# Kernel optimization log

Hardware: AMD Instinct MI355X
Metric: run time of the kernel (lower is better)

## Reference

```python
import jax, jax.numpy as jnp
import numpy as np

B, L, H, T, C = 4, 256, 768, 16, 6
SIM_THR = 0.0
EPS_LN = 1e-5


def layer_norm(x, g, b):
    m = x.mean(-1, keepdims=True)
    v = ((x - m) ** 2).mean(-1, keepdims=True)
    return (x - m) / jnp.sqrt(v + EPS_LN) * g + b


def setup_inputs() -> dict:
    key = jax.random.key(0)
    ks = jax.random.split(key, 20)
    s = 0.02
    embeddings = jax.random.normal(ks[0], (B, L, H), jnp.float32)
    masks = jnp.ones((B, L, L), jnp.float32)
    asp_st = jax.random.randint(ks[1], (B, T), 0, 12)
    asp_ed = asp_st + jax.random.randint(ks[2], (B, T), 0, 3)
    opi_st = jax.random.randint(ks[3], (B, T), 0, 12)
    opi_ed = opi_st + jax.random.randint(ks[4], (B, T), 0, 3)
    sent_id = jax.random.randint(ks[5], (B, T), 2, 5)
    return {
        "embeddings": embeddings, "masks": masks,
        "asp_st": asp_st, "asp_ed": asp_ed, "opi_st": opi_st, "opi_ed": opi_ed,
        "sent_id": sent_id,
        "edge_embed": jax.random.normal(ks[6], (2, H), jnp.float32) * s,
        "W_tp": jax.random.normal(ks[7], (2 * H + 3, H), jnp.float32) * s,
        "b_tp": jnp.zeros((H,), jnp.float32),
        "W_attn": jax.random.normal(ks[8], (3 * H, 1), jnp.float32) * s,
        "b_attn": jnp.zeros((1,), jnp.float32),
        "W_gat": jax.random.normal(ks[9], (2 * H, H), jnp.float32) * s,
        "b_gat": jnp.zeros((H,), jnp.float32),
        "gamma0": jnp.ones((H,), jnp.float32), "beta0": jnp.zeros((H,), jnp.float32),
        "W1": jax.random.normal(ks[10], (2 * H, L), jnp.float32) * s,
        "bl1": jnp.zeros((L,), jnp.float32),
        "gamma1": jnp.ones((L,), jnp.float32), "beta1": jnp.zeros((L,), jnp.float32),
        "Wc": jax.random.normal(ks[11], (L, C), jnp.float32) * s,
        "bc": jnp.zeros((C,), jnp.float32),
        "Wc1": jax.random.normal(ks[12], (L, 2), jnp.float32) * s,
        "bc1": jnp.zeros((2,), jnp.float32),
    }


def _triplet_enhance(emb_b, a_st, a_ed, o_st, o_ed, sid,
                     edge_embed, W_tp, b_tp, W_attn, b_attn, W_gat, b_gat):
    # emb_b: [L,H]; span ints: [T]
    pos = jnp.arange(L)
    am = (pos[None, :] >= a_st[:, None]) & (pos[None, :] <= a_ed[:, None])  # [T,L]
    om = (pos[None, :] >= o_st[:, None]) & (pos[None, :] <= o_ed[:, None])
    amf = am.astype(emb_b.dtype)
    omf = om.astype(emb_b.dtype)
    asp = (amf @ emb_b) / amf.sum(1, keepdims=True)  # [T,H] span-mean
    opi = (omf @ emb_b) / omf.sum(1, keepdims=True)
    sv = jax.nn.one_hot(sid - 2, 3, dtype=emb_b.dtype)  # [T,3]
    nf = jnp.concatenate([asp, opi, sv], -1) @ W_tp + b_tp  # [T,H]

    # cosine similarity between triplet nodes
    nrm = nf / jnp.maximum(jnp.linalg.norm(nf, axis=-1, keepdims=True), 1e-8)
    sim = nrm @ nrm.T
    eye = jnp.eye(T, dtype=bool)
    ok = (sim > SIM_THR) & ~eye
    m0 = ok & (a_st[:, None] == a_st[None, :]) & (a_ed[:, None] == a_ed[None, :])
    m1 = ok & (o_st[:, None] == o_st[None, :]) & (o_ed[:, None] == o_ed[None, :])
    # edge (i,j): src=i, tgt=j -> incoming mask indexed [tgt, src, etype]
    emask = jnp.stack([m0.T, m1.T], axis=-1)  # [T,T,2]

    E = edge_embed  # [2,H]
    cc = jnp.concatenate([
        jnp.broadcast_to(nf[:, None, None, :], (T, T, 2, H)),   # target feats
        jnp.broadcast_to(nf[None, :, None, :], (T, T, 2, H)),   # source feats
        jnp.broadcast_to(E[None, None, :, :], (T, T, 2, H)),
    ], -1)  # [T,T,2,3H]
    scores = (jax.nn.leaky_relu(cc, 0.2) @ W_attn)[..., 0] + b_attn[0]  # [T,T,2]
    neg = jnp.where(emask, scores, -1e9)
    attn = jax.nn.softmax(neg.reshape(T, -1), axis=-1).reshape(T, T, 2)
    msg = jnp.concatenate([
        jnp.broadcast_to(nf[:, None, :], (T, 2, H)),
        jnp.broadcast_to(E[None, :, :], (T, 2, H)),
    ], -1)  # [src, etype, 2H]
    agg = jnp.einsum('tse,sef->tf', attn, msg)
    upd = jax.nn.relu(agg @ W_gat + b_gat)
    has_in = emask.any(axis=(1, 2))
    new_nf = jnp.where(has_in[:, None], upd, nf)
    has_edges = emask.any().astype(emb_b.dtype)  # original skips scatter if no edges
    center = (a_st + o_st) // 2
    return emb_b.at[center].add(new_nf * has_edges)


def reference(embeddings, masks, asp_st, asp_ed, opi_st, opi_ed, sent_id,
              edge_embed, W_tp, b_tp, W_attn, b_attn, W_gat, b_gat,
              gamma0, beta0, W1, bl1, gamma1, beta1, Wc, bc, Wc1, bc1):
    emb1 = layer_norm(embeddings, gamma0, beta0)
    emb = jax.vmap(_triplet_enhance,
                   in_axes=(0, 0, 0, 0, 0, 0) + (None,) * 7)(
        emb1, asp_st, asp_ed, opi_st, opi_ed, sent_id,
        edge_embed, W_tp, b_tp, W_attn, b_attn, W_gat, b_gat)

    # cat([feat_exp, feat_expT]) @ W1  ==  emb@W1[:H] (rows) + emb@W1[H:] (cols)
    A = jnp.einsum('bih,hk->bik', emb, W1[:H])
    Bm = jnp.einsum('bjh,hk->bjk', emb, W1[H:])
    hidden = A[:, :, None, :] + Bm[:, None, :, :] + bl1  # [B,L,L,L]
    hidden = jax.nn.gelu(layer_norm(hidden, gamma1, beta1), approximate=False)
    logits = (hidden @ Wc + bc) * masks[..., None]    # [B,L,L,C]
    logits1 = (hidden @ Wc1 + bc1) * masks[..., None]  # [B,L,L,2]
    return jnp.concatenate([logits, logits1], -1)
```

## Files before the change

kernel.cpp:

```cpp
#include <hip/hip_runtime.h>

__device__ __forceinline__ unsigned short f2bf(float f) {
    union { float f; unsigned u; } v; v.f = f;
    unsigned u = v.u;
    unsigned r = (u + 0x7fffu + ((u >> 16) & 1u)) >> 16;
    return (unsigned short)r;
}
__device__ __forceinline__ float blo(unsigned u) {
    union { unsigned v; float f; } x; x.v = u << 16; return x.f;
}
__device__ __forceinline__ float bhi(unsigned u) {
    union { unsigned v; float f; } x; x.v = u & 0xffff0000u; return x.f;
}

typedef __attribute__((ext_vector_type(8))) short short8;
typedef __attribute__((ext_vector_type(4))) float floatx4;

#define Bn 4
#define Ln 256
#define Hn 768
#define Tn 16

__global__ __launch_bounds__(256) void k_ln0(const float* __restrict__ x,
                                             const float* __restrict__ g,
                                             const float* __restrict__ be,
                                             float* __restrict__ out) {
    int row = blockIdx.x, tid = threadIdx.x;
    const float* xr = x + (size_t)row * Hn;
    float v0 = xr[tid], v1 = xr[tid + 256], v2 = xr[tid + 512];
    float s = v0 + v1 + v2;
    float q = v0 * v0 + v1 * v1 + v2 * v2;
    __shared__ float sm[4], qm[4];
    for (int o = 32; o > 0; o >>= 1) { s += __shfl_down(s, o); q += __shfl_down(q, o); }
    if ((tid & 63) == 0) { sm[tid >> 6] = s; qm[tid >> 6] = q; }
    __syncthreads();
    float S = sm[0] + sm[1] + sm[2] + sm[3];
    float Q = qm[0] + qm[1] + qm[2] + qm[3];
    float mean = S * (1.f / 768.f);
    float rstd = rsqrtf(Q * (1.f / 768.f) - mean * mean + 1e-5f);
    float* o0 = out + (size_t)row * Hn;
    o0[tid]       = (v0 - mean) * rstd * g[tid]       + be[tid];
    o0[tid + 256] = (v1 - mean) * rstd * g[tid + 256] + be[tid + 256];
    o0[tid + 512] = (v2 - mean) * rstd * g[tid + 512] + be[tid + 512];
}

__global__ __launch_bounds__(256) void k_spans(const float* __restrict__ emb,
                                               const int* __restrict__ ast_, const int* __restrict__ aed_,
                                               const int* __restrict__ ost_, const int* __restrict__ oed_,
                                               const int* __restrict__ sid_,
                                               float* __restrict__ xv,
                                               float* __restrict__ nf) {
    int n = blockIdx.x, b = n >> 4, tid = threadIdx.x;
    int ast = ast_[n], aed = aed_[n], ost = ost_[n], oed = oed_[n], sid = sid_[n];
    float ai = 1.f / (float)(aed - ast + 1);
    float oi = 1.f / (float)(oed - ost + 1);
    const float* eb = emb + (size_t)b * Ln * Hn;
    float* xr = xv + (size_t)n * 1568;
    for (int r = tid; r < 1568; r += 256) {
        float v;
        if (r < 768) {
            float s = 0.f;
            for (int l = ast; l <= aed; ++l) s += eb[l * Hn + r];
            v = s * ai;
        } else if (r < 1536) {
            int h = r - 768;
            float s = 0.f;
            for (int l = ost; l <= oed; ++l) s += eb[l * Hn + h];
            v = s * oi;
        } else if (r < 1539) {
            v = (sid - 2 == r - 1536) ? 1.f : 0.f;
        } else {
            v = 0.f;
        }
        xr[r] = v;
    }
    float* nr = nf + (size_t)n * Hn;
    nr[tid] = 0.f; nr[tid + 256] = 0.f; nr[tid + 512] = 0.f;
}

__global__ __launch_bounds__(256) void k_skinny(const float* __restrict__ A,
                                                const float* __restrict__ B,
                                                const float* __restrict__ bias,
                                                float* __restrict__ C,
                                                int Kpad, int Kb, int Kc) {
    __shared__ float At[32][33], Bt[32][33];
    int tid = threadIdx.x;
    int n0 = blockIdx.x * 32, m0 = blockIdx.y * 32, z = blockIdx.z;
    int kbeg = z * Kc;
    int kend = kbeg + Kc; if (kend > Kpad) kend = Kpad;
    int lr = tid >> 3, lc = (tid & 7) * 4;
    int tm = tid >> 3, tn4 = (tid & 7) * 4;
    float acc0 = 0.f, acc1 = 0.f, acc2 = 0.f, acc3 = 0.f;
    for (int k0 = kbeg; k0 < kend; k0 += 32) {
        float4 av = *(const float4*)(A + (size_t)(m0 + lr) * Kpad + k0 + lc);
        At[lr][lc] = av.x; At[lr][lc + 1] = av.y; At[lr][lc + 2] = av.z; At[lr][lc + 3] = av.w;
        int gk = k0 + lr;
        float4 bv = {0.f, 0.f, 0.f, 0.f};
        if (gk < Kb) bv = *(const float4*)(B + (size_t)gk * 768 + n0 + lc);
        Bt[lr][lc] = bv.x; Bt[lr][lc + 1] = bv.y; Bt[lr][lc + 2] = bv.z; Bt[lr][lc + 3] = bv.w;
        __syncthreads();
#pragma unroll
        for (int k = 0; k < 32; ++k) {
            float a = At[tm][k];
            acc0 = fmaf(a, Bt[k][tn4], acc0);
            acc1 = fmaf(a, Bt[k][tn4 + 1], acc1);
            acc2 = fmaf(a, Bt[k][tn4 + 2], acc2);
            acc3 = fmaf(a, Bt[k][tn4 + 3], acc3);
        }
        __syncthreads();
    }
    if (z == 0) {
        acc0 += bias[n0 + tn4];
        acc1 += bias[n0 + tn4 + 1];
        acc2 += bias[n0 + tn4 + 2];
        acc3 += bias[n0 + tn4 + 3];
    }
    float* dst = C + (size_t)(m0 + tm) * 768 + n0 + tn4;
    atomicAdd(&dst[0], acc0);
    atomicAdd(&dst[1], acc1);
    atomicAdd(&dst[2], acc2);
    atomicAdd(&dst[3], acc3);
}

__global__ __launch_bounds__(256) void k_graph(const float* __restrict__ nf,
                                               const int* __restrict__ ast_, const int* __restrict__ aed_,
                                               const int* __restrict__ ost_, const int* __restrict__ oed_,
                                               const float* __restrict__ E,
                                               const float* __restrict__ Wat,
                                               const float* __restrict__ bat,
                                               float* __restrict__ w_out, float* __restrict__ ae_out,
                                               int* __restrict__ hasin, float* __restrict__ hasedge) {
    int b = blockIdx.x, tid = threadIdx.x;
    __shared__ float nfs[16][780];
    __shared__ int ast[16], aed[16], ost[16], oed[16];
    __shared__ float red[256];
    __shared__ float nrm[16], p[16], q[16], rr[2];
    __shared__ unsigned m0b[16], m1b[16];
    const float* nfb = nf + (size_t)b * 16 * Hn;
    for (int e = tid; e < 3072; e += 256) {
        int r = e / 192, c = (e - r * 192) * 4;
        float4 v = *(const float4*)(nfb + r * Hn + c);
        nfs[r][c] = v.x; nfs[r][c + 1] = v.y; nfs[r][c + 2] = v.z; nfs[r][c + 3] = v.w;
    }
    if (tid < 16) {
        int n = b * 16 + tid;
        ast[tid] = ast_[n]; aed[tid] = aed_[n]; ost[tid] = ost_[n]; oed[tid] = oed_[n];
        m0b[tid] = 0u; m1b[tid] = 0u;
    }
    __syncthreads();
    int t = tid >> 4, lane = tid & 15;
    float ss = 0.f, pp = 0.f, qq = 0.f;
    for (int h = lane; h < 768; h += 16) {
        float v = nfs[t][h];
        ss = fmaf(v, v, ss);
        float lr = v > 0.f ? v : 0.2f * v;
        pp = fmaf(lr, Wat[h], pp);
        qq = fmaf(lr, Wat[768 + h], qq);
    }
    red[tid] = ss; __syncthreads();
    if (tid < 16) { float s = 0.f; for (int k2 = 0; k2 < 16; ++k2) s += red[tid * 16 + k2]; nrm[tid] = sqrtf(s); }
    __syncthreads();
    red[tid] = pp; __syncthreads();
    if (tid < 16) { float s = 0.f; for (int k2 = 0; k2 < 16; ++k2) s += red[tid * 16 + k2]; p[tid] = s; }
    __syncthreads();
    red[tid] = qq; __syncthreads();
    if (tid < 16) { float s = 0.f; for (int k2 = 0; k2 < 16; ++k2) s += red[tid * 16 + k2]; q[tid] = s; }
    __syncthreads();
    float rp = 0.f;
    if (tid < 32) {
        int e = tid >> 4;
        for (int h = lane; h < 768; h += 16) {
            float v = E[e * 768 + h];
            float lr = v > 0.f ? v : 0.2f * v;
            rp = fmaf(lr, Wat[1536 + h], rp);
        }
    }
    red[tid] = rp; __syncthreads();
    if (tid < 2) { float s = 0.f; for (int k2 = 0; k2 < 16; ++k2) s += red[tid * 16 + k2]; rr[tid] = s; }
    __syncthreads();
    {
        int i = tid >> 4, j = tid & 15;
        float dot = 0.f;
#pragma unroll 8
        for (int h = 0; h < 768; ++h) dot = fmaf(nfs[i][h], nfs[j][h], dot);
        float sim = dot / (fmaxf(nrm[i], 1e-8f) * fmaxf(nrm[j], 1e-8f));
        bool ok = (sim > 0.f) && (i != j);
        if (ok && ast[i] == ast[j] && aed[i] == aed[j]) atomicOr(&m0b[i], 1u << j);
        if (ok && ost[i] == ost[j] && oed[i] == oed[j]) atomicOr(&m1b[i], 1u << j);
    }
    __syncthreads();
    if (tid < 16) {
        int tt = tid;
        float battn = bat[0];
        float sc[32];
        float mx = -3.4e38f;
        bool hi = false;
#pragma unroll
        for (int s = 0; s < 16; ++s) {
            bool e0 = (m0b[s] >> tt) & 1u;
            bool e1 = (m1b[s] >> tt) & 1u;
            float base = p[tt] + q[s] + battn;
            float v0 = e0 ? (base + rr[0]) : -1e9f;
            float v1 = e1 ? (base + rr[1]) : -1e9f;
            sc[2 * s] = v0; sc[2 * s + 1] = v1;
            mx = fmaxf(mx, fmaxf(v0, v1));
            hi = hi || e0 || e1;
        }
        float sum = 0.f;
#pragma unroll
        for (int k2 = 0; k2 < 32; ++k2) { float e = expf(sc[k2] - mx); sc[k2] = e; sum += e; }
        float inv = 1.f / sum;
        float ae0 = 0.f, ae1 = 0.f;
#pragma unroll
        for (int s = 0; s < 16; ++s) {
            float w0 = sc[2 * s] * inv, w1 = sc[2 * s + 1] * inv;
            w_out[(size_t)(b * 16 + tt) * 16 + s] = w0 + w1;
            ae0 += w0; ae1 += w1;
        }
        ae_out[(b * 16 + tt) * 2 + 0] = ae0;
        ae_out[(b * 16 + tt) * 2 + 1] = ae1;
        hasin[b * 16 + tt] = hi ? 1 : 0;
        red[tid] = hi ? 1.f : 0.f;
    }
    __syncthreads();
    if (tid == 0) {
        float he = 0.f;
        for (int k2 = 0; k2 < 16; ++k2) he = fmaxf(he, red[k2]);
        hasedge[b] = he;
    }
}

__global__ __launch_bounds__(256) void k_agg(const float* __restrict__ nf,
                                             const float* __restrict__ w, const float* __restrict__ ae,
                                             const float* __restrict__ E,
                                             float* __restrict__ agg,
                                             float* __restrict__ raw) {
    int n = blockIdx.x, b = n >> 4, tid = threadIdx.x;
    __shared__ float nfs[16][768];
    __shared__ float ws[16];
    const float* nfb = nf + (size_t)b * 16 * Hn;
    for (int e = tid; e < 3072; e += 256) {
        int r = e / 192, c = (e - r * 192) * 4;
        *(float4*)&nfs[r][c] = *(const float4*)(nfb + r * Hn + c);
    }
    if (tid < 16) ws[tid] = w[(size_t)n * 16 + tid];
    __syncthreads();
    float ae0 = ae[2 * n], ae1 = ae[2 * n + 1];
    float* ag = agg + (size_t)n * 1536;
    for (int f = tid; f < 768; f += 256) {
        float s = 0.f;
#pragma unroll
        for (int s16 = 0; s16 < 16; ++s16) s = fmaf(ws[s16], nfs[s16][f], s);
        ag[f] = s;
        ag[768 + f] = ae0 * E[f] + ae1 * E[768 + f];
    }
    float* rr = raw + (size_t)n * Hn;
    rr[tid] = 0.f; rr[tid + 256] = 0.f; rr[tid + 512] = 0.f;
}

__global__ __launch_bounds__(256) void k_scatter(const float* __restrict__ raw,
                                                 const float* __restrict__ nf,
                                                 const int* __restrict__ hasin, const float* __restrict__ hasedge,
                                                 const int* __restrict__ ast_, const int* __restrict__ ost_,
                                                 float* __restrict__ emb) {
    int n = blockIdx.x, b = n >> 4, tid = threadIdx.x;
    if (hasedge[b] == 0.f) return;
    int center = (ast_[n] + ost_[n]) >> 1;
    float* dst = emb + (size_t)(b * Ln + center) * Hn;
    int hi = hasin[n];
    const float* src = hi ? (raw + (size_t)n * Hn) : (nf + (size_t)n * Hn);
    for (int h = tid; h < 768; h += 256) {
        float v = src[h];
        if (hi) v = fmaxf(v, 0.f);
        atomicAdd(&dst[h], v);
    }
}

__global__ __launch_bounds__(256) void k_cvt(const float* __restrict__ in,
                                             unsigned short* __restrict__ out) {
    int i = (blockIdx.x * 256 + threadIdx.x) * 4;
    float4 v = *(const float4*)(in + i);
    ushort4 o;
    o.x = f2bf(v.x); o.y = f2bf(v.y); o.z = f2bf(v.z); o.w = f2bf(v.w);
    *(ushort4*)(out + i) = o;
}

__global__ __launch_bounds__(256) void k_w1t(const float* __restrict__ W1,
                                             unsigned short* __restrict__ w1t) {
    __shared__ float tile[32][33];
    int kt = blockIdx.x, nt = blockIdx.y, tid = threadIdx.x;
    int k0 = kt * 32, n0 = nt * 32;
    int rowoff = (n0 < 256) ? 0 : 768;
    int col0 = n0 & 255;
    int r = tid >> 3, c = (tid & 7) * 4;
    float4 v = *(const float4*)(W1 + (size_t)(rowoff + k0 + r) * 256 + col0 + c);
    tile[r][c] = v.x; tile[r][c + 1] = v.y; tile[r][c + 2] = v.z; tile[r][c + 3] = v.w;
    __syncthreads();
    ushort4 o;
    o.x = f2bf(tile[c][r]); o.y = f2bf(tile[c + 1][r]);
    o.z = f2bf(tile[c + 2][r]); o.w = f2bf(tile[c + 3][r]);
    *(ushort4*)(w1t + (size_t)(n0 + r) * 768 + k0 + c) = o;
}

__global__ __launch_bounds__(64) void k_gemm(const unsigned short* __restrict__ embh,
                                             const unsigned short* __restrict__ w1t,
                                             float* __restrict__ abm) {
    int wid = blockIdx.x;
    int m0 = (wid >> 4) * 32;
    int n0 = (wid & 15) * 32;
    int lane = threadIdx.x;
    int r = lane & 15, g = lane >> 4;
    const short8* Ap0 = (const short8*)(embh + (size_t)(m0 + r) * 768 + g * 8);
    const short8* Ap1 = (const short8*)(embh + (size_t)(m0 + 16 + r) * 768 + g * 8);
    const short8* Bp0 = (const short8*)(w1t + (size_t)(n0 + r) * 768 + g * 8);
    const short8* Bp1 = (const short8*)(w1t + (size_t)(n0 + 16 + r) * 768 + g * 8);
    floatx4 acc00 = {0.f, 0.f, 0.f, 0.f}, acc01 = {0.f, 0.f, 0.f, 0.f};
    floatx4 acc10 = {0.f, 0.f, 0.f, 0.f}, acc11 = {0.f, 0.f, 0.f, 0.f};
#pragma unroll 4
    for (int ks = 0; ks < 768; ks += 32) {
        short8 a0 = Ap0[ks >> 3];
        short8 a1 = Ap1[ks >> 3];
        short8 b0 = Bp0[ks >> 3];
        short8 b1 = Bp1[ks >> 3];
        acc00 = __builtin_amdgcn_mfma_f32_16x16x32_bf16(a0, b0, acc00, 0, 0, 0);
        acc01 = __builtin_amdgcn_mfma_f32_16x16x32_bf16(a0, b1, acc01, 0, 0, 0);
        acc10 = __builtin_amdgcn_mfma_f32_16x16x32_bf16(a1, b0, acc10, 0, 0, 0);
        acc11 = __builtin_amdgcn_mfma_f32_16x16x32_bf16(a1, b1, acc11, 0, 0, 0);
    }
#pragma unroll
    for (int t = 0; t < 4; ++t) {
        int row = g * 4 + t;
        abm[(size_t)(m0 + row) * 512 + n0 + r]           = acc00[t];
        abm[(size_t)(m0 + row) * 512 + n0 + 16 + r]      = acc01[t];
        abm[(size_t)(m0 + 16 + row) * 512 + n0 + r]      = acc10[t];
        abm[(size_t)(m0 + 16 + row) * 512 + n0 + 16 + r] = acc11[t];
    }
}

__global__ __launch_bounds__(256) void k_hidden(const float* __restrict__ abm,
                                                const float* __restrict__ masks,
                                                const float* __restrict__ bl1,
                                                const float* __restrict__ g1,
                                                const float* __restrict__ b1,
                                                const float* __restrict__ Wc,
                                                const float* __restrict__ bc,
                                                const float* __restrict__ Wc1,
                                                const float* __restrict__ bc1,
                                                float* __restrict__ out) {
    __shared__ __align__(16) float As[32][260];
    __shared__ __align__(16) float Bs[16][260];
    __shared__ __align__(16) float g1s[256];
    __shared__ __align__(16) float b1s[256];
    __shared__ __align__(16) unsigned short wch[256][8];
    __shared__ float bcs[8];
    int tid = threadIdx.x;
    int jt = blockIdx.x, it = blockIdx.y, b = blockIdx.z;
    const float* Ag = abm + (size_t)(b * 256 + it * 32) * 512;
    const float* Bg = abm + (size_t)(b * 256 + jt * 16) * 512 + 256;
#pragma unroll
    for (int u = 0; u < 32; ++u) {
        As[u][tid] = Ag[u * 512 + tid];
    }
#pragma unroll
    for (int u = 0; u < 16; ++u) {
        Bs[u][tid] = Bg[u * 512 + tid] + bl1[tid];
    }
    g1s[tid] = g1[tid];
    b1s[tid] = b1[tid];
    {
        int k = tid;
#pragma unroll
        for (int c = 0; c < 6; ++c) wch[k][c] = f2bf(Wc[k * 6 + c]);
        wch[k][6] = f2bf(Wc1[k * 2]);
        wch[k][7] = f2bf(Wc1[k * 2 + 1]);
    }
    if (tid < 6) bcs[tid] = bc[tid];
    else if (tid < 8) bcs[tid] = bc1[tid - 6];
    __syncthreads();

    int i0 = (tid >> 4) * 2;
    int jl = tid & 15;
    const float4* Ar0 = (const float4*)As[i0];
    const float4* Ar1 = (const float4*)As[i0 + 1];
    const float4* Br  = (const float4*)Bs[jl];
    const float4* G4  = (const float4*)g1s;
    const float4* Bb4 = (const float4*)b1s;
    const uint4*  W4  = (const uint4*)wch;

    float s0 = 0.f, q0 = 0.f, s1 = 0.f, q1 = 0.f;
#pragma unroll 8
    for (int kq = 0; kq < 64; ++kq) {
        float4 a0 = Ar0[kq], a1 = Ar1[kq], bv = Br[kq];
        float h;
        h = a0.x + bv.x; s0 += h; q0 = fmaf(h, h, q0);
        h = a0.y + bv.y; s0 += h; q0 = fmaf(h, h, q0);
        h = a0.z + bv.z; s0 += h; q0 = fmaf(h, h, q0);
        h = a0.w + bv.w; s0 += h; q0 = fmaf(h, h, q0);
        h = a1.x + bv.x; s1 += h; q1 = fmaf(h, h, q1);
        h = a1.y + bv.y; s1 += h; q1 = fmaf(h, h, q1);
        h = a1.z + bv.z; s1 += h; q1 = fmaf(h, h, q1);
        h = a1.w + bv.w; s1 += h; q1 = fmaf(h, h, q1);
    }
    const float inv256 = 1.f / 256.f;
    float mn0 = s0 * inv256, mn1 = s1 * inv256;
    float r0 = rsqrtf(q0 * inv256 - mn0 * mn0 + 1e-5f);
    float r1 = rsqrtf(q1 * inv256 - mn1 * mn1 + 1e-5f);
    float c0 = -mn0 * r0, c1 = -mn1 * r1;

    float acc0[8], acc1[8];
#pragma unroll
    for (int c = 0; c < 8; ++c) { acc0[c] = 0.f; acc1[c] = 0.f; }

    const float K1 = -1.5957691216f, K2 = -0.0713548163f;

#define STEP(AE0, AE1, BE, GE, BBE, WIDX) do {                                   \
        float h0 = (AE0) + (BE);                                                 \
        float x0 = fmaf(h0, r0, c0); x0 = fmaf(x0, (GE), (BBE));                 \
        float m0_ = fmaf(x0 * x0, K2, K1);                                       \
        float e0 = __expf(x0 * m0_);                                             \
        float y0 = x0 * __builtin_amdgcn_rcpf(1.f + e0);                         \
        float h1 = (AE1) + (BE);                                                 \
        float x1 = fmaf(h1, r1, c1); x1 = fmaf(x1, (GE), (BBE));                 \
        float m1_ = fmaf(x1 * x1, K2, K1);                                       \
        float e1 = __expf(x1 * m1_);                                             \
        float y1 = x1 * __builtin_amdgcn_rcpf(1.f + e1);                         \
        uint4 wv = W4[WIDX];                                                     \
        float w_0 = blo(wv.x), w_1 = bhi(wv.x), w_2 = blo(wv.y), w_3 = bhi(wv.y);\
        float w_4 = blo(wv.z), w_5 = bhi(wv.z), w_6 = blo(wv.w), w_7 = bhi(wv.w);\
        acc0[0] = fmaf(y0, w_0, acc0[0]); acc1[0] = fmaf(y1, w_0, acc1[0]);      \
        acc0[1] = fmaf(y0, w_1, acc0[1]); acc1[1] = fmaf(y1, w_1, acc1[1]);      \
        acc0[2] = fmaf(y0, w_2, acc0[2]); acc1[2] = fmaf(y1, w_2, acc1[2]);      \
        acc0[3] = fmaf(y0, w_3, acc0[3]); acc1[3] = fmaf(y1, w_3, acc1[3]);      \
        acc0[4] = fmaf(y0, w_4, acc0[4]); acc1[4] = fmaf(y1, w_4, acc1[4]);      \
        acc0[5] = fmaf(y0, w_5, acc0[5]); acc1[5] = fmaf(y1, w_5, acc1[5]);      \
        acc0[6] = fmaf(y0, w_6, acc0[6]); acc1[6] = fmaf(y1, w_6, acc1[6]);      \
        acc0[7] = fmaf(y0, w_7, acc0[7]); acc1[7] = fmaf(y1, w_7, acc1[7]);      \
    } while (0)

#pragma unroll 4
    for (int kq = 0; kq < 64; ++kq) {
        float4 a0 = Ar0[kq], a1 = Ar1[kq], bv = Br[kq];
        float4 g4 = G4[kq], bb4 = Bb4[kq];
        STEP(a0.x, a1.x, bv.x, g4.x, bb4.x, 4 * kq + 0);
        STEP(a0.y, a1.y, bv.y, g4.y, bb4.y, 4 * kq + 1);
        STEP(a0.z, a1.z, bv.z, g4.z, bb4.z, 4 * kq + 2);
        STEP(a0.w, a1.w, bv.w, g4.w, bb4.w, 4 * kq + 3);
    }
#undef STEP

    int i = it * 32 + i0;
    int j = jt * 16 + jl;
    float mk0 = masks[(size_t)(b * 256 + i) * 256 + j];
    float mk1 = masks[(size_t)(b * 256 + i + 1) * 256 + j];
    float* dst0 = out + ((size_t)(b * 256 + i) * 256 + j) * 8;
    float* dst1 = out + ((size_t)(b * 256 + i + 1) * 256 + j) * 8;
    float4 oA, oB;
    oA.x = (acc0[0] + bcs[0]) * mk0; oA.y = (acc0[1] + bcs[1]) * mk0;
    oA.z = (acc0[2] + bcs[2]) * mk0; oA.w = (acc0[3] + bcs[3]) * mk0;
    oB.x = (acc0[4] + bcs[4]) * mk0; oB.y = (acc0[5] + bcs[5]) * mk0;
    oB.z = (acc0[6] + bcs[6]) * mk0; oB.w = (acc0[7] + bcs[7]) * mk0;
    *(float4*)(dst0)     = oA;
    *(float4*)(dst0 + 4) = oB;
    oA.x = (acc1[0] + bcs[0]) * mk1; oA.y = (acc1[1] + bcs[1]) * mk1;
    oA.z = (acc1[2] + bcs[2]) * mk1; oA.w = (acc1[3] + bcs[3]) * mk1;
    oB.x = (acc1[4] + bcs[4]) * mk1; oB.y = (acc1[5] + bcs[5]) * mk1;
    oB.z = (acc1[6] + bcs[6]) * mk1; oB.w = (acc1[7] + bcs[7]) * mk1;
    *(float4*)(dst1)     = oA;
    *(float4*)(dst1 + 4) = oB;
}

extern "C" void kernel_launch(void* const* d_in, const int* in_sizes, int n_in,
                              void* d_out, int out_size, void* d_ws, size_t ws_size,
                              hipStream_t stream) {
    (void)in_sizes; (void)n_in; (void)out_size; (void)ws_size;
    const float* emb_in = (const float*)d_in[0];
    const float* masks  = (const float*)d_in[1];
    const int* ast = (const int*)d_in[2];
    const int* aed = (const int*)d_in[3];
    const int* ost = (const int*)d_in[4];
    const int* oed = (const int*)d_in[5];
    const int* sid = (const int*)d_in[6];
    const float* E    = (const float*)d_in[7];
    const float* Wtp  = (const float*)d_in[8];
    const float* btp  = (const float*)d_in[9];
    const float* Wat  = (const float*)d_in[10];
    const float* bat  = (const float*)d_in[11];
    const float* Wg   = (const float*)d_in[12];
    const float* bg   = (const float*)d_in[13];
    const float* g0   = (const float*)d_in[14];
    const float* b0   = (const float*)d_in[15];
    const float* W1   = (const float*)d_in[16];
    const float* bl1  = (const float*)d_in[17];
    const float* g1   = (const float*)d_in[18];
    const float* b1   = (const float*)d_in[19];
    const float* Wc   = (const float*)d_in[20];
    const float* bc   = (const float*)d_in[21];
    const float* Wc1  = (const float*)d_in[22];
    const float* bc1  = (const float*)d_in[23];
    float* outp = (float*)d_out;

    float* fw = (float*)d_ws;
    float* emb = fw;
    float* nf  = emb + 786432;
    float* wts = nf + 49152;
    float* ae  = wts + 1024;
    int*   hasin = (int*)(ae + 128);
    float* hasedge = (float*)(hasin + 64);
    float* xv  = fw + 836864;
    float* agg = fw + 937216;
    float* raw = fw + 1035520;
    float* abm = fw + 1084672;
    unsigned short* embh = (unsigned short*)(fw + 1608960);
    unsigned short* w1t  = (unsigned short*)(fw + 2002176);

    dim3 gw(24, 16);
    k_w1t<<<gw, 256, 0, stream>>>(W1, w1t);
    k_ln0<<<1024, 256, 0, stream>>>(emb_in, g0, b0, emb);
    k_spans<<<64, 256, 0, stream>>>(emb, ast, aed, ost, oed, sid, xv, nf);
    dim3 gs1(24, 2, 4);
    k_skinny<<<gs1, 256, 0, stream>>>(xv, Wtp, btp, nf, 1568, 1539, 416);
    k_graph<<<4, 256, 0, stream>>>(nf, ast, aed, ost, oed, E, Wat, bat, wts, ae, hasin, hasedge);
    k_agg<<<64, 256, 0, stream>>>(nf, wts, ae, E, agg, raw);
    k_skinny<<<gs1, 256, 0, stream>>>(agg, Wg, bg, raw, 1536, 1536, 384);
    k_scatter<<<64, 256, 0, stream>>>(raw, nf, hasin, hasedge, ast, ost, emb);
    k_cvt<<<768, 256, 0, stream>>>(emb, embh);
    k_gemm<<<512, 64, 0, stream>>>(embh, w1t, abm);
    dim3 g6(16, 8, 4);
    k_hidden<<<g6, 256, 0, stream>>>(abm, masks, bl1, g1, b1, Wc, bc, Wc1, bc1, outp);
}
```

Before: 253.9 us.

## Use MFMA for the hidden classifier and precompute LayerNorm statistics algebraically

The dominant hidden kernel is rewritten so the 256-wide GELU output goes through bf16 MFMA against packed Wc/Wc1 weights instead of scalar FMAs. The per-pair LayerNorm mean and variance come from precomputed row sums, sums of squares and an A·B dot-product matrix, computed by new prep and dots kernels, so the kernel no longer makes a separate reduction pass over hidden. The agg kernel is merged into k_graph, the bf16 conversion kernel is folded into the GEMM's A-operand load, and the split-K count of k_skinny changes. This trades a bf16 rounding of A, B, gamma/beta and activations for tensor-core throughput, and the variance formula E[x²]−mu² risks cancellation error.

```diff
diff --git a/kernel.cpp b/kernel.cpp
--- a/kernel.cpp
+++ b/kernel.cpp
@@ -6,11 +6,8 @@
     unsigned r = (u + 0x7fffu + ((u >> 16) & 1u)) >> 16;
     return (unsigned short)r;
 }
-__device__ __forceinline__ float blo(unsigned u) {
-    union { unsigned v; float f; } x; x.v = u << 16; return x.f;
-}
-__device__ __forceinline__ float bhi(unsigned u) {
-    union { unsigned v; float f; } x; x.v = u & 0xffff0000u; return x.f;
+__device__ __forceinline__ float bfup(int x) {
+    union { unsigned u; float f; } v; v.u = ((unsigned)(unsigned short)x) << 16; return v.f;
 }
 
 typedef __attribute__((ext_vector_type(8))) short short8;
@@ -128,13 +125,16 @@
                                                const float* __restrict__ E,
                                                const float* __restrict__ Wat,
                                                const float* __restrict__ bat,
-                                               float* __restrict__ w_out, float* __restrict__ ae_out,
-                                               int* __restrict__ hasin, float* __restrict__ hasedge) {
+                                               int* __restrict__ hasin, float* __restrict__ hasedge,
+                                               float* __restrict__ agg, float* __restrict__ raw) {
     int b = blockIdx.x, tid = threadIdx.x;
     __shared__ float nfs[16][780];
+    __shared__ float Es[2][768];
     __shared__ int ast[16], aed[16], ost[16], oed[16];
     __shared__ float red[256];
     __shared__ float nrm[16], p[16], q[16], rr[2];
+    __shared__ float ws2[16][16];
+    __shared__ float aes[16][2];
     __shared__ unsigned m0b[16], m1b[16];
     const float* nfb = nf + (size_t)b * 16 * Hn;
     for (int e = tid; e < 3072; e += 256) {
@@ -142,6 +142,7 @@
         float4 v = *(const float4*)(nfb + r * Hn + c);
         nfs[r][c] = v.x; nfs[r][c + 1] = v.y; nfs[r][c + 2] = v.z; nfs[r][c + 3] = v.w;
     }
+    for (int e = tid; e < 1536; e += 256) ((float*)Es)[e] = E[e];
     if (tid < 16) {
         int n = b * 16 + tid;
         ast[tid] = ast_[n]; aed[tid] = aed_[n]; ost[tid] = ost_[n]; oed[tid] = oed_[n];
@@ -170,7 +171,7 @@
     if (tid < 32) {
         int e = tid >> 4;
         for (int h = lane; h < 768; h += 16) {
-            float v = E[e * 768 + h];
+            float v = Es[e][h];
             float lr = v > 0.f ? v : 0.2f * v;
             rp = fmaf(lr, Wat[1536 + h], rp);
         }
@@ -180,9 +181,15 @@
     __syncthreads();
     {
         int i = tid >> 4, j = tid & 15;
+        const float4* ri = (const float4*)nfs[i];
+        const float4* rj = (const float4*)nfs[j];
         float dot = 0.f;
-#pragma unroll 8
-        for (int h = 0; h < 768; ++h) dot = fmaf(nfs[i][h], nfs[j][h], dot);
+#pragma unroll 4
+        for (int h4 = 0; h4 < 192; ++h4) {
+            float4 a = ri[h4], c = rj[h4];
+            dot = fmaf(a.x, c.x, dot); dot = fmaf(a.y, c.y, dot);
+            dot = fmaf(a.z, c.z, dot); dot = fmaf(a.w, c.w, dot);
+        }
         float sim = dot / (fmaxf(nrm[i], 1e-8f) * fmaxf(nrm[j], 1e-8f));
         bool ok = (sim > 0.f) && (i != j);
         if (ok && ast[i] == ast[j] && aed[i] == aed[j]) atomicOr(&m0b[i], 1u << j);
@@ -214,11 +221,10 @@
 #pragma unroll
         for (int s = 0; s < 16; ++s) {
             float w0 = sc[2 * s] * inv, w1 = sc[2 * s + 1] * inv;
-            w_out[(size_t)(b * 16 + tt) * 16 + s] = w0 + w1;
+            ws2[tt][s] = w0 + w1;
             ae0 += w0; ae1 += w1;
         }
-        ae_out[(b * 16 + tt) * 2 + 0] = ae0;
-        ae_out[(b * 16 + tt) * 2 + 1] = ae1;
+        aes[tt][0] = ae0; aes[tt][1] = ae1;
         hasin[b * 16 + tt] = hi ? 1 : 0;
         red[tid] = hi ? 1.f : 0.f;
     }
@@ -228,34 +234,20 @@
         for (int k2 = 0; k2 < 16; ++k2) he = fmaxf(he, red[k2]);
         hasedge[b] = he;
     }
-}
-
-__global__ __launch_bounds__(256) void k_agg(const float* __restrict__ nf,
-                                             const float* __restrict__ w, const float* __restrict__ ae,
-                                             const float* __restrict__ E,
-                                             float* __restrict__ agg,
-                                             float* __restrict__ raw) {
-    int n = blockIdx.x, b = n >> 4, tid = threadIdx.x;
-    __shared__ float nfs[16][768];
-    __shared__ float ws[16];
-    const float* nfb = nf + (size_t)b * 16 * Hn;
-    for (int e = tid; e < 3072; e += 256) {
-        int r = e / 192, c = (e - r * 192) * 4;
-        *(float4*)&nfs[r][c] = *(const float4*)(nfb + r * Hn + c);
-    }
-    if (tid < 16) ws[tid] = w[(size_t)n * 16 + tid];
-    __syncthreads();
-    float ae0 = ae[2 * n], ae1 = ae[2 * n + 1];
-    float* ag = agg + (size_t)n * 1536;
-    for (int f = tid; f < 768; f += 256) {
-        float s = 0.f;
-#pragma unroll
-        for (int s16 = 0; s16 < 16; ++s16) s = fmaf(ws[s16], nfs[s16][f], s);
-        ag[f] = s;
-        ag[768 + f] = ae0 * E[f] + ae1 * E[768 + f];
-    }
-    float* rr = raw + (size_t)n * Hn;
-    rr[tid] = 0.f; rr[tid + 256] = 0.f; rr[tid + 512] = 0.f;
+    for (int nn = 0; nn < 16; ++nn) {
+        int n = b * 16 + nn;
+        float ae0 = aes[nn][0], ae1 = aes[nn][1];
+        float* ag = agg + (size_t)n * 1536;
+        float* rw = raw + (size_t)n * Hn;
+        for (int f = tid; f < 768; f += 256) {
+            float s = 0.f;
+#pragma unroll
+            for (int s16 = 0; s16 < 16; ++s16) s = fmaf(ws2[nn][s16], nfs[s16][f], s);
+            ag[f] = s;
+            ag[768 + f] = ae0 * Es[0][f] + ae1 * Es[1][f];
+            rw[f] = 0.f;
+        }
+    }
 }
 
 __global__ __launch_bounds__(256) void k_scatter(const float* __restrict__ raw,
@@ -276,15 +268,6 @@
     }
 }
 
-__global__ __launch_bounds__(256) void k_cvt(const float* __restrict__ in,
-                                             unsigned short* __restrict__ out) {
-    int i = (blockIdx.x * 256 + threadIdx.x) * 4;
-    float4 v = *(const float4*)(in + i);
-    ushort4 o;
-    o.x = f2bf(v.x); o.y = f2bf(v.y); o.z = f2bf(v.z); o.w = f2bf(v.w);
-    *(ushort4*)(out + i) = o;
-}
-
 __global__ __launch_bounds__(256) void k_w1t(const float* __restrict__ W1,
                                              unsigned short* __restrict__ w1t) {
     __shared__ float tile[32][33];
@@ -302,7 +285,7 @@
     *(ushort4*)(w1t + (size_t)(n0 + r) * 768 + k0 + c) = o;
 }
 
-__global__ __launch_bounds__(64) void k_gemm(const unsigned short* __restrict__ embh,
+__global__ __launch_bounds__(64) void k_gemm(const float* __restrict__ emb,
                                              const unsigned short* __restrict__ w1t,
                                              float* __restrict__ abm) {
     int wid = blockIdx.x;
@@ -310,16 +293,26 @@
     int n0 = (wid & 15) * 32;
     int lane = threadIdx.x;
     int r = lane & 15, g = lane >> 4;
-    const short8* Ap0 = (const short8*)(embh + (size_t)(m0 + r) * 768 + g * 8);
-    const short8* Ap1 = (const short8*)(embh + (size_t)(m0 + 16 + r) * 768 + g * 8);
+    const float* Af0 = emb + (size_t)(m0 + r) * 768 + g * 8;
+    const float* Af1 = emb + (size_t)(m0 + 16 + r) * 768 + g * 8;
     const short8* Bp0 = (const short8*)(w1t + (size_t)(n0 + r) * 768 + g * 8);
     const short8* Bp1 = (const short8*)(w1t + (size_t)(n0 + 16 + r) * 768 + g * 8);
     floatx4 acc00 = {0.f, 0.f, 0.f, 0.f}, acc01 = {0.f, 0.f, 0.f, 0.f};
     floatx4 acc10 = {0.f, 0.f, 0.f, 0.f}, acc11 = {0.f, 0.f, 0.f, 0.f};
 #pragma unroll 4
     for (int ks = 0; ks < 768; ks += 32) {
-        short8 a0 = Ap0[ks >> 3];
-        short8 a1 = Ap1[ks >> 3];
+        float4 x0 = *(const float4*)(Af0 + ks);
+        float4 x1 = *(const float4*)(Af0 + ks + 4);
+        float4 y0 = *(const float4*)(Af1 + ks);
+        float4 y1 = *(const float4*)(Af1 + ks + 4);
+        short8 a0, a1;
+        union { float f; unsigned u; } cv;
+#define PK(dst, idx, val) { cv.f = (val); dst[idx] = (short)((cv.u + 0x8000u) >> 16); }
+        PK(a0, 0, x0.x) PK(a0, 1, x0.y) PK(a0, 2, x0.z) PK(a0, 3, x0.w)
+        PK(a0, 4, x1.x) PK(a0, 5, x1.y) PK(a0, 6, x1.z) PK(a0, 7, x1.w)
+        PK(a1, 0, y0.x) PK(a1, 1, y0.y) PK(a1, 2, y0.z) PK(a1, 3, y0.w)
+        PK(a1, 4, y1.x) PK(a1, 5, y1.y) PK(a1, 6, y1.z) PK(a1, 7, y1.w)
+#undef PK
         short8 b0 = Bp0[ks >> 3];
         short8 b1 = Bp1[ks >> 3];
         acc00 = __builtin_amdgcn_mfma_f32_16x16x32_bf16(a0, b0, acc00, 0, 0, 0);
@@ -337,136 +330,171 @@
     }
 }
 
-__global__ __launch_bounds__(256) void k_hidden(const float* __restrict__ abm,
-                                                const float* __restrict__ masks,
-                                                const float* __restrict__ bl1,
-                                                const float* __restrict__ g1,
-                                                const float* __restrict__ b1,
-                                                const float* __restrict__ Wc,
-                                                const float* __restrict__ bc,
-                                                const float* __restrict__ Wc1,
-                                                const float* __restrict__ bc1,
-                                                float* __restrict__ out) {
-    __shared__ __align__(16) float As[32][260];
-    __shared__ __align__(16) float Bs[16][260];
-    __shared__ __align__(16) float g1s[256];
-    __shared__ __align__(16) float b1s[256];
-    __shared__ __align__(16) unsigned short wch[256][8];
-    __shared__ float bcs[8];
+__global__ __launch_bounds__(256) void k_prep(const float* __restrict__ abm,
+                                              const float* __restrict__ bl1,
+                                              unsigned short* __restrict__ Abf,
+                                              unsigned short* __restrict__ Bbf,
+                                              float* __restrict__ sA, float* __restrict__ qA,
+                                              float* __restrict__ sB, float* __restrict__ qB) {
+    int rw = blockIdx.x, tid = threadIdx.x;
+    float a = abm[(size_t)rw * 512 + tid];
+    float bp = abm[(size_t)rw * 512 + 256 + tid] + bl1[tid];
+    Abf[(size_t)rw * 256 + tid] = f2bf(a);
+    Bbf[(size_t)rw * 256 + tid] = f2bf(bp);
+    float v0 = a, v1 = a * a, v2 = bp, v3 = bp * bp;
+    __shared__ float red[4][4];
+    for (int o = 32; o > 0; o >>= 1) {
+        v0 += __shfl_down(v0, o); v1 += __shfl_down(v1, o);
+        v2 += __shfl_down(v2, o); v3 += __shfl_down(v3, o);
+    }
+    if ((tid & 63) == 0) {
+        int w = tid >> 6;
+        red[w][0] = v0; red[w][1] = v1; red[w][2] = v2; red[w][3] = v3;
+    }
+    __syncthreads();
+    if (tid == 0) {
+        sA[rw] = red[0][0] + red[1][0] + red[2][0] + red[3][0];
+        qA[rw] = red[0][1] + red[1][1] + red[2][1] + red[3][1];
+        sB[rw] = red[0][2] + red[1][2] + red[2][2] + red[3][2];
+        qB[rw] = red[0][3] + red[1][3] + red[2][3] + red[3][3];
+    }
+}
+
+__global__ __launch_bounds__(256) void k_dots(const float* __restrict__ abm,
+                                              const float* __restrict__ bl1,
+                                              float* __restrict__ D) {
+    __shared__ float At[32][33], Bt[32][33];
+    int tid = threadIdx.x;
+    int j0 = blockIdx.x * 32, i0 = blockIdx.y * 32, b = blockIdx.z;
+    int lr = tid >> 3, lc = (tid & 7) * 4;
+    int ti = tid >> 3, tj4 = (tid & 7) * 4;
+    float acc0 = 0.f, acc1 = 0.f, acc2 = 0.f, acc3 = 0.f;
+    for (int k0 = 0; k0 < 256; k0 += 32) {
+        float4 av = *(const float4*)(abm + (size_t)(b * 256 + i0 + lr) * 512 + k0 + lc);
+        At[lr][lc] = av.x; At[lr][lc + 1] = av.y; At[lr][lc + 2] = av.z; At[lr][lc + 3] = av.w;
+        float4 bv = *(const float4*)(abm + (size_t)(b * 256 + j0 + lr) * 512 + 256 + k0 + lc);
+        float4 lv = *(const float4*)(bl1 + k0 + lc);
+        Bt[lr][lc] = bv.x + lv.x; Bt[lr][lc + 1] = bv.y + lv.y;
+        Bt[lr][lc + 2] = bv.z + lv.z; Bt[lr][lc + 3] = bv.w + lv.w;
+        __syncthreads();
+#pragma unroll
+        for (int k = 0; k < 32; ++k) {
+            float a = At[ti][k];
+            acc0 = fmaf(a, Bt[tj4][k], acc0);
+            acc1 = fmaf(a, Bt[tj4 + 1][k], acc1);
+            acc2 = fmaf(a, Bt[tj4 + 2][k], acc2);
+            acc3 = fmaf(a, Bt[tj4 + 3][k], acc3);
+        }
+        __syncthreads();
+    }
+    float* dst = D + ((size_t)b * 256 + i0 + ti) * 256 + j0 + tj4;
+    dst[0] = acc0; dst[1] = acc1; dst[2] = acc2; dst[3] = acc3;
+}
+
+__global__ __launch_bounds__(256) void k_hidden2(const unsigned short* __restrict__ Abf,
+                                                 const unsigned short* __restrict__ Bbf,
+                                                 const float* __restrict__ sA, const float* __restrict__ qA,
+                                                 const float* __restrict__ sB, const float* __restrict__ qB,
+                                                 const float* __restrict__ D,
+                                                 const float* __restrict__ masks,
+                                                 const float* __restrict__ g1, const float* __restrict__ b1,
+                                                 const float* __restrict__ Wc, const float* __restrict__ bc,
+                                                 const float* __restrict__ Wc1, const float* __restrict__ bc1,
+                                                 float* __restrict__ out) {
+    __shared__ unsigned short As[16][272];
+    __shared__ unsigned short Bs[16][272];
+    __shared__ unsigned short gsh[256], bsh[256];
+    __shared__ short8 Wf[8][64];
+    __shared__ float Ds[16][16];
+    __shared__ float ms[16][16];
+    __shared__ float sAs[16], qAs[16], sBs[16], qBs[16];
     int tid = threadIdx.x;
     int jt = blockIdx.x, it = blockIdx.y, b = blockIdx.z;
-    const float* Ag = abm + (size_t)(b * 256 + it * 32) * 512;
-    const float* Bg = abm + (size_t)(b * 256 + jt * 16) * 512 + 256;
-#pragma unroll
-    for (int u = 0; u < 32; ++u) {
-        As[u][tid] = Ag[u * 512 + tid];
-    }
-#pragma unroll
-    for (int u = 0; u < 16; ++u) {
-        Bs[u][tid] = Bg[u * 512 + tid] + bl1[tid];
-    }
-    g1s[tid] = g1[tid];
-    b1s[tid] = b1[tid];
+    int rowA = b * 256 + it * 16;
+    int rowB = b * 256 + jt * 16;
+#pragma unroll
+    for (int u = 0; u < 2; ++u) {
+        int e = tid + u * 256;
+        int r = e >> 5, ch = e & 31;
+        *(short8*)&As[r][ch * 8] = *(const short8*)(Abf + (size_t)(rowA + r) * 256 + ch * 8);
+        *(short8*)&Bs[r][ch * 8] = *(const short8*)(Bbf + (size_t)(rowB + r) * 256 + ch * 8);
+    }
+    gsh[tid] = f2bf(g1[tid]);
+    bsh[tid] = f2bf(b1[tid]);
+#pragma unroll
+    for (int u = 0; u < 2; ++u) {
+        int e = tid + u * 256;
+        int s = e >> 6, l = e & 63;
+        int qq2 = l >> 4, nn2 = l & 15;
+        short8 wv;
+#pragma unroll
+        for (int t = 0; t < 8; ++t) {
+            int k = s * 32 + qq2 * 8 + t;
+            float v = (nn2 < 6) ? Wc[k * 6 + nn2] : ((nn2 < 8) ? Wc1[k * 2 + (nn2 - 6)] : 0.f);
+            wv[t] = (short)f2bf(v);
+        }
+        Wf[s][l] = wv;
+    }
     {
-        int k = tid;
-#pragma unroll
-        for (int c = 0; c < 6; ++c) wch[k][c] = f2bf(Wc[k * 6 + c]);
-        wch[k][6] = f2bf(Wc1[k * 2]);
-        wch[k][7] = f2bf(Wc1[k * 2 + 1]);
-    }
-    if (tid < 6) bcs[tid] = bc[tid];
-    else if (tid < 8) bcs[tid] = bc1[tid - 6];
-    __syncthreads();
-
-    int i0 = (tid >> 4) * 2;
-    int jl = tid & 15;
-    const float4* Ar0 = (const float4*)As[i0];
-    const float4* Ar1 = (const float4*)As[i0 + 1];
-    const float4* Br  = (const float4*)Bs[jl];
-    const float4* G4  = (const float4*)g1s;
-    const float4* Bb4 = (const float4*)b1s;
-    const uint4*  W4  = (const uint4*)wch;
-
-    float s0 = 0.f, q0 = 0.f, s1 = 0.f, q1 = 0.f;
-#pragma unroll 8
-    for (int kq = 0; kq < 64; ++kq) {
-        float4 a0 = Ar0[kq], a1 = Ar1[kq], bv = Br[kq];
-        float h;
-        h = a0.x + bv.x; s0 += h; q0 = fmaf(h, h, q0);
-        h = a0.y + bv.y; s0 += h; q0 = fmaf(h, h, q0);
-        h = a0.z + bv.z; s0 += h; q0 = fmaf(h, h, q0);
-        h = a0.w + bv.w; s0 += h; q0 = fmaf(h, h, q0);
-        h = a1.x + bv.x; s1 += h; q1 = fmaf(h, h, q1);
-        h = a1.y + bv.y; s1 += h; q1 = fmaf(h, h, q1);
-        h = a1.z + bv.z; s1 += h; q1 = fmaf(h, h, q1);
-        h = a1.w + bv.w; s1 += h; q1 = fmaf(h, h, q1);
-    }
+        int di = tid >> 4, dj = tid & 15;
+        size_t gi = ((size_t)(b * 256 + it * 16 + di)) * 256 + jt * 16 + dj;
+        Ds[di][dj] = D[gi];
+        ms[di][dj] = masks[gi];
+    }
+    if (tid < 16) {
+        sAs[tid] = sA[rowA + tid]; qAs[tid] = qA[rowA + tid];
+        sBs[tid] = sB[rowB + tid]; qBs[tid] = qB[rowB + tid];
+    }
+    __syncthreads();
+
+    int lane = tid & 63, w = tid >> 6;
+    int m = lane & 15, q = lane >> 4;
+    int iA = w * 4 + (m & 3);
+    int n = m;
+    float bcs_l = (n < 6) ? bc[n] : ((n < 8) ? bc1[n - 6] : 0.f);
     const float inv256 = 1.f / 256.f;
-    float mn0 = s0 * inv256, mn1 = s1 * inv256;
-    float r0 = rsqrtf(q0 * inv256 - mn0 * mn0 + 1e-5f);
-    float r1 = rsqrtf(q1 * inv256 - mn1 * mn1 + 1e-5f);
-    float c0 = -mn0 * r0, c1 = -mn1 * r1;
-
-    float acc0[8], acc1[8];
-#pragma unroll
-    for (int c = 0; c < 8; ++c) { acc0[c] = 0.f; acc1[c] = 0.f; }
-
     const float K1 = -1.5957691216f, K2 = -0.0713548163f;
 
-#define STEP(AE0, AE1, BE, GE, BBE, WIDX) do {                                   \
-        float h0 = (AE0) + (BE);                                                 \
-        float x0 = fmaf(h0, r0, c0); x0 = fmaf(x0, (GE), (BBE));                 \
-        float m0_ = fmaf(x0 * x0, K2, K1);                                       \
-        float e0 = __expf(x0 * m0_);                                             \
-        float y0 = x0 * __builtin_amdgcn_rcpf(1.f + e0);                         \
-        float h1 = (AE1) + (BE);                                                 \
-        float x1 = fmaf(h1, r1, c1); x1 = fmaf(x1, (GE), (BBE));                 \
-        float m1_ = fmaf(x1 * x1, K2, K1);                                       \
-        float e1 = __expf(x1 * m1_);                                             \
-        float y1 = x1 * __builtin_amdgcn_rcpf(1.f + e1);                         \
-        uint4 wv = W4[WIDX];                                                     \
-        float w_0 = blo(wv.x), w_1 = bhi(wv.x), w_2 = blo(wv.y), w_3 = bhi(wv.y);\
-        float w_4 = blo(wv.z), w_5 = bhi(wv.z), w_6 = blo(wv.w), w_7 = bhi(wv.w);\
-        acc0[0] = fmaf(y0, w_0, acc0[0]); acc1[0] = fmaf(y1, w_0, acc1[0]);      \
-        acc0[1] = fmaf(y0, w_1, acc0[1]); acc1[1] = fmaf(y1, w_1, acc1[1]);      \
-        acc0[2] = fmaf(y0, w_2, acc0[2]); acc1[2] = fmaf(y1, w_2, acc1[2]);      \
-        acc0[3] = fmaf(y0, w_3, acc0[3]); acc1[3] = fmaf(y1, w_3, acc1[3]);      \
-        acc0[4] = fmaf(y0, w_4, acc0[4]); acc1[4] = fmaf(y1, w_4, acc1[4]);      \
-        acc0[5] = fmaf(y0, w_5, acc0[5]); acc1[5] = fmaf(y1, w_5, acc1[5]);      \
-        acc0[6] = fmaf(y0, w_6, acc0[6]); acc1[6] = fmaf(y1, w_6, acc1[6]);      \
-        acc0[7] = fmaf(y0, w_7, acc0[7]); acc1[7] = fmaf(y1, w_7, acc1[7]);      \
-    } while (0)
-
-#pragma unroll 4
-    for (int kq = 0; kq < 64; ++kq) {
-        float4 a0 = Ar0[kq], a1 = Ar1[kq], bv = Br[kq];
-        float4 g4 = G4[kq], bb4 = Bb4[kq];
-        STEP(a0.x, a1.x, bv.x, g4.x, bb4.x, 4 * kq + 0);
-        STEP(a0.y, a1.y, bv.y, g4.y, bb4.y, 4 * kq + 1);
-        STEP(a0.z, a1.z, bv.z, g4.z, bb4.z, 4 * kq + 2);
-        STEP(a0.w, a1.w, bv.w, g4.w, bb4.w, 4 * kq + 3);
-    }
-#undef STEP
-
-    int i = it * 32 + i0;
-    int j = jt * 16 + jl;
-    float mk0 = masks[(size_t)(b * 256 + i) * 256 + j];
-    float mk1 = masks[(size_t)(b * 256 + i + 1) * 256 + j];
-    float* dst0 = out + ((size_t)(b * 256 + i) * 256 + j) * 8;
-    float* dst1 = out + ((size_t)(b * 256 + i + 1) * 256 + j) * 8;
-    float4 oA, oB;
-    oA.x = (acc0[0] + bcs[0]) * mk0; oA.y = (acc0[1] + bcs[1]) * mk0;
-    oA.z = (acc0[2] + bcs[2]) * mk0; oA.w = (acc0[3] + bcs[3]) * mk0;
-    oB.x = (acc0[4] + bcs[4]) * mk0; oB.y = (acc0[5] + bcs[5]) * mk0;
-    oB.z = (acc0[6] + bcs[6]) * mk0; oB.w = (acc0[7] + bcs[7]) * mk0;
-    *(float4*)(dst0)     = oA;
-    *(float4*)(dst0 + 4) = oB;
-    oA.x = (acc1[0] + bcs[0]) * mk1; oA.y = (acc1[1] + bcs[1]) * mk1;
-    oA.z = (acc1[2] + bcs[2]) * mk1; oA.w = (acc1[3] + bcs[3]) * mk1;
-    oB.x = (acc1[4] + bcs[4]) * mk1; oB.y = (acc1[5] + bcs[5]) * mk1;
-    oB.z = (acc1[6] + bcs[6]) * mk1; oB.w = (acc1[7] + bcs[7]) * mk1;
-    *(float4*)(dst1)     = oA;
-    *(float4*)(dst1 + 4) = oB;
+    for (int p = 0; p < 4; ++p) {
+        int jB = p * 4 + (m >> 2);
+        float mu = (sAs[iA] + sBs[jB]) * inv256;
+        float E2 = (qAs[iA] + 2.f * Ds[iA][jB] + qBs[jB]) * inv256;
+        float r_ = rsqrtf(E2 - mu * mu + 1e-5f);
+        float c_ = -mu * r_;
+        floatx4 acc = {0.f, 0.f, 0.f, 0.f};
+#pragma unroll
+        for (int s = 0; s < 8; ++s) {
+            int ko = s * 32 + q * 8;
+            short8 a8 = *(const short8*)&As[iA][ko];
+            short8 b8 = *(const short8*)&Bs[jB][ko];
+            short8 g8 = *(const short8*)&gsh[ko];
+            short8 v8 = *(const short8*)&bsh[ko];
+            short8 yv;
+#pragma unroll
+            for (int t = 0; t < 8; ++t) {
+                float h = bfup(a8[t]) + bfup(b8[t]);
+                float x = fmaf(h, r_, c_);
+                x = fmaf(x, bfup(g8[t]), bfup(v8[t]));
+                float mm = fmaf(x * x, K2, K1);
+                float e = __expf(x * mm);
+                float y = x * __builtin_amdgcn_rcpf(1.f + e);
+                union { float f; unsigned u; } cv; cv.f = y;
+                yv[t] = (short)((cv.u + 0x8000u) >> 16);
+            }
+            acc = __builtin_amdgcn_mfma_f32_16x16x32_bf16(yv, Wf[s][lane], acc, 0, 0, 0);
+        }
+        if (n < 8) {
+#pragma unroll
+            for (int rg = 0; rg < 4; ++rg) {
+                int mp = q * 4 + rg;
+                int il = w * 4 + (mp & 3);
+                int jl = p * 4 + (mp >> 2);
+                float mk = ms[il][jl];
+                size_t idx = (((size_t)(b * 256 + it * 16 + il)) * 256 + jt * 16 + jl) * 8 + n;
+                out[idx] = (acc[rg] + bcs_l) * mk;
+            }
+        }
+    }
 }
 
 extern "C" void kernel_launch(void* const* d_in, const int* in_sizes, int n_in,
@@ -501,30 +529,36 @@
 
     float* fw = (float*)d_ws;
     float* emb = fw;
-    float* nf  = emb + 786432;
-    float* wts = nf + 49152;
-    float* ae  = wts + 1024;
-    int*   hasin = (int*)(ae + 128);
-    float* hasedge = (float*)(hasin + 64);
-    float* xv  = fw + 836864;
-    float* agg = fw + 937216;
-    float* raw = fw + 1035520;
-    float* abm = fw + 1084672;
-    unsigned short* embh = (unsigned short*)(fw + 1608960);
-    unsigned short* w1t  = (unsigned short*)(fw + 2002176);
+    float* nf  = fw + 786432;
+    int*   hasin = (int*)(fw + 835584);
+    float* hasedge = fw + 835648;
+    float* xv  = fw + 835712;
+    float* agg = fw + 936064;
+    float* raw = fw + 1034368;
+    float* Dd  = fw + 835712;
+    float* abm = fw + 1097856;
+    float* sA  = fw + 1622144;
+    float* qA  = fw + 1623168;
+    float* sB  = fw + 1624192;
+    float* qB  = fw + 1625216;
+    unsigned short* Abf = (unsigned short*)(fw + 1626240);
+    unsigned short* Bbf = (unsigned short*)(fw + 1757312);
+    unsigned short* w1t = (unsigned short*)(fw + 1888384);
 
     dim3 gw(24, 16);
     k_w1t<<<gw, 256, 0, stream>>>(W1, w1t);
     k_ln0<<<1024, 256, 0, stream>>>(emb_in, g0, b0, emb);
     k_spans<<<64, 256, 0, stream>>>(emb, ast, aed, ost, oed, sid, xv, nf);
-    dim3 gs1(24, 2, 4);
-    k_skinny<<<gs1, 256, 0, stream>>>(xv, Wtp, btp, nf, 1568, 1539, 416);
-    k_graph<<<4, 256, 0, stream>>>(nf, ast, aed, ost, oed, E, Wat, bat, wts, ae, hasin, hasedge);
-    k_agg<<<64, 256, 0, stream>>>(nf, wts, ae, E, agg, raw);
-    k_skinny<<<gs1, 256, 0, stream>>>(agg, Wg, bg, raw, 1536, 1536, 384);
+    dim3 gs1(24, 2, 7);
+    k_skinny<<<gs1, 256, 0, stream>>>(xv, Wtp, btp, nf, 1568, 1539, 224);
+    k_graph<<<4, 256, 0, stream>>>(nf, ast, aed, ost, oed, E, Wat, bat, hasin, hasedge, agg, raw);
+    k_skinny<<<gs1, 256, 0, stream>>>(agg, Wg, bg, raw, 1536, 1536, 224);
     k_scatter<<<64, 256, 0, stream>>>(raw, nf, hasin, hasedge, ast, ost, emb);
-    k_cvt<<<768, 256, 0, stream>>>(emb, embh);
-    k_gemm<<<512, 64, 0, stream>>>(embh, w1t, abm);
-    dim3 g6(16, 8, 4);
-    k_hidden<<<g6, 256, 0, stream>>>(abm, masks, bl1, g1, b1, Wc, bc, Wc1, bc1, outp);
-}
+    k_gemm<<<512, 64, 0, stream>>>(emb, w1t, abm);
+    k_prep<<<1024, 256, 0, stream>>>(abm, bl1, Abf, Bbf, sA, qA, sB, qB);
+    dim3 gd(8, 8, 4);
+    k_dots<<<gd, 256, 0, stream>>>(abm, bl1, Dd);
+    dim3 g6(16, 16, 4);
+    k_hidden2<<<g6, 256, 0, stream>>>(Abf, Bbf, sA, qA, sB, qB, Dd, masks,
+                                      g1, b1, Wc, bc, Wc1, bc1, outp);
+}
```

Measured after the change: 265.7 us. 1.05x slower.
